# Kernel tuning notes

Hardware: AMD Instinct MI355X
Metric: run time of the kernel (lower is better)

## Reference

```python
import jax, jax.numpy as jnp
import numpy as np

VOCAB, D, S, T, B, E, C = 21128, 768, 50, 5, 512, 128, 10


def gcn(x, edges, W, b):
    # GCNConv with self-loops and symmetric normalization. x: [S, D]
    N = x.shape[0]
    loop = jnp.arange(N)
    src = jnp.concatenate([edges[0], loop])
    dst = jnp.concatenate([edges[1], loop])
    deg = jax.ops.segment_sum(jnp.ones_like(src, dtype=x.dtype), dst, num_segments=N)
    dinv = jax.lax.rsqrt(jnp.maximum(deg, 1e-12))
    norm = dinv[src] * dinv[dst]
    h = x @ W  # [S, 10]
    out = jax.ops.segment_sum(h[src] * norm[:, None], dst, num_segments=N)
    return out + b


def mpm(self_f, cross_f, assign, W1, b1, W2, b2):
    # multi-perspective matching, broadcast over leading dims; node dim = -2
    a = assign * self_f
    c = assign * cross_f
    num = jnp.sum(a * c, axis=-1)
    den = jnp.maximum(jnp.linalg.norm(a, axis=-1) * jnp.linalg.norm(c, axis=-1), 1e-8)
    cos = num / den
    bshape = jnp.broadcast_shapes(self_f.shape[:-2], cross_f.shape[:-2])
    sf = jnp.broadcast_to(self_f, bshape + self_f.shape[-2:])
    h = jnp.concatenate([cos[..., None], sf], axis=-1)  # [..., S, 11]
    h = jax.nn.relu(h @ W1 + b1) @ W2 + b2  # [..., S, 20]
    return jnp.max(h, axis=-2)  # [..., 20]


def setup_inputs() -> dict:
    key = jax.random.key(0)
    ks = jax.random.split(key, 20)
    inp = {
        "context_input": jax.random.randint(ks[0], (B, T, S), 0, VOCAB),
        "response_input": jax.random.randint(ks[1], (B, S), 0, VOCAB),
        "context_graph_adjs": jax.random.randint(ks[2], (B, T, 2, E), 0, S),
        "response_graph_adj": jax.random.randint(ks[3], (B, 2, E), 0, S),
        "word_emb": jax.random.normal(ks[4], (VOCAB, D), jnp.float32) * 0.02,
        "conv_W": jax.random.normal(ks[5], (D, C), jnp.float32) * 0.05,
        "conv_b": jnp.zeros((C,), jnp.float32),
        "cross_w": jax.random.uniform(ks[6], (D, C), jnp.float32),
        "attention_coef": jax.random.uniform(ks[7], (S, S), jnp.float32),
        "assign_weight": jax.random.uniform(ks[8], (S, C), jnp.float32),
        "mp_W1": jax.random.normal(ks[9], (C + 1, 20), jnp.float32) * 0.3,
        "mp_b1": jnp.zeros((20,), jnp.float32),
        "mp_W2": jax.random.normal(ks[10], (20, 20), jnp.float32) * 0.2,
        "mp_b2": jnp.zeros((20,), jnp.float32),
        "ffn_W1": jax.random.normal(ks[11], (80, 40), jnp.float32) * 0.1,
        "ffn_b1": jnp.zeros((40,), jnp.float32),
        "ffn_W2": jax.random.normal(ks[12], (40, 1), jnp.float32) * 0.2,
        "ffn_b2": jnp.zeros((1,), jnp.float32),
    }
    return inp


def reference(context_input, response_input, context_graph_adjs, response_graph_adj,
              word_emb, conv_W, conv_b, cross_w, attention_coef, assign_weight,
              mp_W1, mp_b1, mp_W2, mp_b2, ffn_W1, ffn_b1, ffn_W2, ffn_b2):
    ctx = word_emb[context_input]      # [B, T, S, D]
    resp = word_emb[response_input]    # [B, S, D]

    gcn_b = jax.vmap(gcn, in_axes=(0, 0, None, None))
    resp_gcn = gcn_b(resp, response_graph_adj, conv_W, conv_b)                      # [B, S, C]
    ctx_gcn = jax.vmap(gcn_b, in_axes=(0, 0, None, None))(ctx, context_graph_adjs, conv_W, conv_b)  # [B, T, S, C]

    # cross features: utterance cross comes from response, response cross from utterance
    u_cross = jnp.einsum('ps,bsk->bpk', attention_coef, resp @ cross_w)   # [B, S, C]
    r_cross = jnp.einsum('ps,btsk->btpk', attention_coef, ctx @ cross_w)  # [B, T, S, C]

    g_u = mpm(ctx_gcn, u_cross[:, None], assign_weight, mp_W1, mp_b1, mp_W2, mp_b2)       # [B, T, 20]
    g_r = mpm(resp_gcn[:, None], r_cross, assign_weight, mp_W1, mp_b1, mp_W2, mp_b2)      # [B, T, 20]

    feat = jnp.concatenate([g_u, g_r, g_u * g_r, jnp.abs(g_u - g_r)], axis=-1)  # [B, T, 80]
    logits = jax.nn.relu(feat @ ffn_W1 + ffn_b1) @ ffn_W2 + ffn_b2              # [B, T, 1]
    return jax.nn.sigmoid(jnp.sum(logits, axis=1))                              # [B, 1]
```

## Files before the change

### kernel.cpp

```cpp
#include <hip/hip_runtime.h>
#include <math.h>

#define VOCAB 21128
#define DD 768
#define SS 50
#define TT 5
#define BB 512
#define EE 128
#define CC 10
#define V20 (VOCAB * 20)
#define NG 2560
#define NALL 3072

__global__ void k_prep(const float* __restrict__ att, float* __restrict__ attG) {
    int i = blockIdx.x * 64 + threadIdx.x;
    if (i < SS * SS) {
        int p = i / SS, s = i - p * SS;
        attG[s * 52 + p] = att[i];
    }
}

__global__ __launch_bounds__(512) void k_vocab(const float* __restrict__ emb,
                                               const float* __restrict__ Wconv,
                                               const float* __restrict__ Wcross,
                                               float* __restrict__ hvp) {
    __shared__ float tile[8][64][21];
    const int wv = threadIdx.x >> 6, lane = threadIdx.x & 63;
    const int rowbase = blockIdx.x * 64;
    const int rsub = lane >> 2, m = lane & 3;

    const int d0w = blockIdx.y * 384 + __builtin_amdgcn_readfirstlane(wv * 48);

    float4 v[12];
#pragma unroll
    for (int ch = 0; ch < 3; ++ch) {
#pragma unroll
        for (int it = 0; it < 4; ++it) {
            int row = it * 16 + rsub;
            long r = rowbase + row;
            if (r >= VOCAB) r = VOCAB - 1;
            v[ch * 4 + it] = *(const float4*)(emb + r * DD + d0w + ch * 16 + m * 4);
        }
    }

    float acc[20];
#pragma unroll
    for (int c = 0; c < 20; c++) acc[c] = 0.f;

#pragma unroll
    for (int ch = 0; ch < 3; ++ch) {
        const int d0 = d0w + ch * 16;
#pragma unroll
        for (int it = 0; it < 4; ++it) {
            const int row = it * 16 + rsub;
            const float4 w = v[ch * 4 + it];
            tile[wv][row][m * 4 + 0] = w.x;
            tile[wv][row][m * 4 + 1] = w.y;
            tile[wv][row][m * 4 + 2] = w.z;
            tile[wv][row][m * 4 + 3] = w.w;
        }
#pragma unroll
        for (int d = 0; d < 16; ++d) {
            float e = tile[wv][lane][d];
            const float* wc = Wconv + (d0 + d) * 10;
            const float* wx = Wcross + (d0 + d) * 10;
#pragma unroll
            for (int c = 0; c < 10; c++) {
                acc[c] = fmaf(e, wc[c], acc[c]);
                acc[10 + c] = fmaf(e, wx[c], acc[10 + c]);
            }
        }
    }

    __syncthreads();
    float* pp = &tile[0][0][0];
#pragma unroll
    for (int c = 0; c < 20; c++) pp[wv * 1280 + lane * 20 + c] = acc[c];
    __syncthreads();
    float* outp = hvp + (long)blockIdx.y * V20;
    for (int i = threadIdx.x; i < 1280; i += 512) {
        int row = i / 20;
        long r = rowbase + row;
        if (r < VOCAB) {
            float s = 0.f;
#pragma unroll
            for (int w = 0; w < 8; ++w) s += pp[w * 1280 + i];
            outp[r * 20 + (i - row * 20)] = s;
        }
    }
}

__global__ __launch_bounds__(256) void k_gcn(const int* __restrict__ ctok,
                                             const int* __restrict__ cadj,
                                             const int* __restrict__ rtok,
                                             const int* __restrict__ radj,
                                             const float* __restrict__ hvp,
                                             const float* __restrict__ convb,
                                             const float* __restrict__ attG,
                                             float* __restrict__ P) {
    __shared__ float hcv[4][SS][12];
    __shared__ float hcx[4][SS][12];
    __shared__ float aggL[4][SS][11];
    __shared__ int dgS[4][64];
    const int tid = threadIdx.x, wv = tid >> 6, lane = tid & 63;
    const int G = blockIdx.x * 4 + wv;

    const int* tb;
    const int* ab;
    if (G < NG) { tb = ctok + (long)G * SS; ab = cadj + (long)G * 2 * EE; }
    else        { int b = G - NG; tb = rtok + (long)b * SS; ab = radj + (long)b * 2 * EE; }

    const int e1s = ab[lane], e2s = ab[lane + 64];
    const int e1d = ab[EE + lane], e2d = ab[EE + lane + 64];
    const int myTok = (lane < SS) ? tb[lane] : 0;

    dgS[wv][lane] = 0;
    atomicAdd(&dgS[wv][e1d], 1);
    atomicAdd(&dgS[wv][e2d], 1);

    const float4* hv4 = (const float4*)hvp;
#pragma unroll
    for (int it = 0; it < 4; ++it) {
        const int idx = it * 64 + lane;
        int row = idx / 5;
        const int q = idx - row * 5;
        const int rowc = (row < SS) ? row : (SS - 1);
        const int t = __shfl(myTok, rowc);
        if (idx < SS * 5) {
            const float4 a = hv4[(long)t * 5 + q];
            const float4 b = hv4[(long)(VOCAB * 5) + (long)t * 5 + q];
            const float4 w = make_float4(a.x + b.x, a.y + b.y, a.z + b.z, a.w + b.w);
            if (q == 0)      *(float4*)&hcv[wv][row][0] = w;
            else if (q == 1) *(float4*)&hcv[wv][row][4] = w;
            else if (q == 2) { hcv[wv][row][8] = w.x; hcv[wv][row][9] = w.y;
                               hcx[wv][row][0] = w.z; hcx[wv][row][1] = w.w; }
            else if (q == 3) { *(float2*)&hcx[wv][row][2] = make_float2(w.x, w.y);
                               *(float2*)&hcx[wv][row][4] = make_float2(w.z, w.w); }
            else             { *(float2*)&hcx[wv][row][6] = make_float2(w.x, w.y);
                               *(float2*)&hcx[wv][row][8] = make_float2(w.z, w.w); }
        }
    }

    float dv = 0.f;
    if (lane < SS) dv = rsqrtf((float)(dgS[wv][lane] + 1));

    float* aggW = &aggL[wv][0][0];
    for (int i = lane; i < SS * 11; i += 64) aggW[i] = 0.f;
    const float n1 = __shfl(dv, e1s) * __shfl(dv, e1d);
    const float n2 = __shfl(dv, e2s) * __shfl(dv, e2d);
#pragma unroll
    for (int c = 0; c < CC; c++) atomicAdd(&aggW[e1d * 11 + c], hcv[wv][e1s][c] * n1);
#pragma unroll
    for (int c = 0; c < CC; c++) atomicAdd(&aggW[e2d * 11 + c], hcv[wv][e2s][c] * n2);

    const int pc = (lane < SS) ? lane : (SS - 1);
    float xo[CC];
#pragma unroll
    for (int c = 0; c < CC; c++) xo[c] = hcx[wv][pc][c];

    const int p = lane;
    if (p < SS) {
        float gcn[CC];
        const float dp2 = dv * dv;
        const float4 s0 = *(const float4*)&hcv[wv][p][0];
        const float4 s1 = *(const float4*)&hcv[wv][p][4];
        const float s8 = hcv[wv][p][8], s9 = hcv[wv][p][9];
        gcn[0] = aggW[p * 11 + 0] + s0.x * dp2 + convb[0];
        gcn[1] = aggW[p * 11 + 1] + s0.y * dp2 + convb[1];
        gcn[2] = aggW[p * 11 + 2] + s0.z * dp2 + convb[2];
        gcn[3] = aggW[p * 11 + 3] + s0.w * dp2 + convb[3];
        gcn[4] = aggW[p * 11 + 4] + s1.x * dp2 + convb[4];
        gcn[5] = aggW[p * 11 + 5] + s1.y * dp2 + convb[5];
        gcn[6] = aggW[p * 11 + 6] + s1.z * dp2 + convb[6];
        gcn[7] = aggW[p * 11 + 7] + s1.w * dp2 + convb[7];
        gcn[8] = aggW[p * 11 + 8] + s8 * dp2 + convb[8];
        gcn[9] = aggW[p * 11 + 9] + s9 * dp2 + convb[9];

        float ax[CC];
#pragma unroll
        for (int c = 0; c < CC; c++) ax[c] = 0.f;
#pragma unroll 5
        for (int s = 0; s < SS; ++s) {
            const float a = attG[s * 52 + p];
#pragma unroll
            for (int c = 0; c < CC; c++) {
                const float xs = __uint_as_float(
                    __builtin_amdgcn_readlane(__float_as_uint(xo[c]), s));
                ax[c] = fmaf(a, xs, ax[c]);
            }
        }
        float4* o4 = (float4*)(P + (long)G * 1000 + p * 20);
        o4[0] = make_float4(gcn[0], gcn[1], gcn[2], gcn[3]);
        o4[1] = make_float4(gcn[4], gcn[5], gcn[6], gcn[7]);
        o4[2] = make_float4(gcn[8], gcn[9], ax[0], ax[1]);
        o4[3] = make_float4(ax[2], ax[3], ax[4], ax[5]);
        o4[4] = make_float4(ax[6], ax[7], ax[8], ax[9]);
    }
}

__global__ __launch_bounds__(640) void k_mpmf(const float* __restrict__ P,
                                              const float* __restrict__ assign,
                                              const float* __restrict__ W1, const float* __restrict__ b1,
                                              const float* __restrict__ W2, const float* __restrict__ b2,
                                              const float* __restrict__ fW1, const float* __restrict__ fb1,
                                              const float* __restrict__ fW2, const float* __restrict__ fb2,
                                              float* __restrict__ out) {
    __shared__ float W2T[20][21];
    __shared__ float asgL[SS][11];
    __shared__ float h1L[10][SS][20];
    __shared__ float guS[TT][20];
    __shared__ float grS[TT][20];
    __shared__ float fsum[256];
    const int tid = threadIdx.x, wv = tid >> 6, lane = tid & 63;
    const int b = blockIdx.x;
    const int t = wv >> 1, which = wv & 1;
    const int g = b * TT + t;

    for (int i = tid; i < 400; i += 640) W2T[i % 20][i / 20] = W2[i];
    for (int i = tid; i < SS * CC; i += 640) asgL[i / CC][i % CC] = assign[i];
    __syncthreads();

    const float* Pc = P + (long)g * 1000;
    const float* Pr = P + (long)(NG + b) * 1000;
    const float* selfP = which ? Pr : Pc;
    const float* croP  = which ? Pc : Pr;

    const int p = lane;
    float self[CC], cro[CC];
    if (p < SS) {
        const float4* s4 = (const float4*)(selfP + p * 20);
        const float4 a0 = s4[0], a1 = s4[1], a2 = s4[2];
        self[0] = a0.x; self[1] = a0.y; self[2] = a0.z; self[3] = a0.w;
        self[4] = a1.x; self[5] = a1.y; self[6] = a1.z; self[7] = a1.w;
        self[8] = a2.x; self[9] = a2.y;
        const float4* c4 = (const float4*)(croP + p * 20);
        const float4 b0 = c4[2], b1q = c4[3], b2q = c4[4];
        cro[0] = b0.z; cro[1] = b0.w;
        cro[2] = b1q.x; cro[3] = b1q.y; cro[4] = b1q.z; cro[5] = b1q.w;
        cro[6] = b2q.x; cro[7] = b2q.y; cro[8] = b2q.z; cro[9] = b2q.w;
    }

    const int j = lane % 20;
    const int grp = lane / 20;
    float w2r[20];
#pragma unroll
    for (int k = 0; k < 20; k++) w2r[k] = W2T[j][k];

    if (p < SS) {
        float num = 0.f, na = 0.f, nc2 = 0.f;
#pragma unroll
        for (int c = 0; c < CC; c++) {
            float av = asgL[p][c];
            float a = av * self[c];
            float cx = av * cro[c];
            num = fmaf(a, cx, num);
            na = fmaf(a, a, na);
            nc2 = fmaf(cx, cx, nc2);
        }
        float cosv = num / fmaxf(sqrtf(na) * sqrtf(nc2), 1e-8f);
        float h1[20];
#pragma unroll
        for (int q = 0; q < 20; q++) h1[q] = fmaf(cosv, W1[q], b1[q]);
#pragma unroll
        for (int k = 0; k < CC; k++) {
            float sv = self[k];
#pragma unroll
            for (int q = 0; q < 20; q++) h1[q] = fmaf(sv, W1[(k + 1) * 20 + q], h1[q]);
        }
        float4* hw = (float4*)&h1L[wv][p][0];
        hw[0] = make_float4(fmaxf(h1[0], 0.f), fmaxf(h1[1], 0.f), fmaxf(h1[2], 0.f), fmaxf(h1[3], 0.f));
        hw[1] = make_float4(fmaxf(h1[4], 0.f), fmaxf(h1[5], 0.f), fmaxf(h1[6], 0.f), fmaxf(h1[7], 0.f));
        hw[2] = make_float4(fmaxf(h1[8], 0.f), fmaxf(h1[9], 0.f), fmaxf(h1[10], 0.f), fmaxf(h1[11], 0.f));
        hw[3] = make_float4(fmaxf(h1[12], 0.f), fmaxf(h1[13], 0.f), fmaxf(h1[14], 0.f), fmaxf(h1[15], 0.f));
        hw[4] = make_float4(fmaxf(h1[16], 0.f), fmaxf(h1[17], 0.f), fmaxf(h1[18], 0.f), fmaxf(h1[19], 0.f));
    }

    float part = -1e30f;
    if (grp < 3) {
        const int s0 = grp * 17;
        const int s1 = (grp == 2) ? SS : (s0 + 17);
        for (int s = s0; s < s1; ++s) {
            const float* hr = &h1L[wv][s][0];
            float tt = 0.f;
#pragma unroll
            for (int k = 0; k < 20; k++) tt = fmaf(hr[k], w2r[k], tt);
            part = fmaxf(part, tt);
        }
    }
    const float a0 = __shfl(part, j);
    const float a1 = __shfl(part, j + 20);
    const float a2 = __shfl(part, j + 40);
    if (lane < 20) {
        float h2 = fmaxf(fmaxf(a0, a1), a2) + b2[lane];
        (which ? grS[t] : guS[t])[lane] = h2;
    }
    __syncthreads();

    float term = 0.f;
    if (tid < 200) {
        const int tt = tid / 40, jj = tid - tt * 40;
        float hvv = fb1[jj];
#pragma unroll
        for (int k = 0; k < 20; k++) {
            float u = guS[tt][k], r = grS[tt][k];
            hvv = fmaf(u, fW1[k * 40 + jj], hvv);
            hvv = fmaf(r, fW1[(20 + k) * 40 + jj], hvv);
            hvv = fmaf(u * r, fW1[(40 + k) * 40 + jj], hvv);
            hvv = fmaf(fabsf(u - r), fW1[(60 + k) * 40 + jj], hvv);
        }
        term = fmaxf(hvv, 0.f) * fW2[jj];
    }
    if (tid < 256) fsum[tid] = term;
    __syncthreads();
    if (wv == 0) {
        float s = fsum[lane] + fsum[lane + 64] + fsum[lane + 128] + fsum[lane + 192];
#pragma unroll
        for (int o = 32; o; o >>= 1) s += __shfl_xor(s, o);
        if (lane == 0) out[b] = 1.f / (1.f + expf(-(s + (float)TT * fb2[0])));
    }
}

extern "C" void kernel_launch(void* const* d_in, const int* in_sizes, int n_in,
                              void* d_out, int out_size, void* d_ws, size_t ws_size,
                              hipStream_t stream) {
    (void)in_sizes; (void)n_in; (void)out_size; (void)ws_size;
    const int* ctx_tok = (const int*)d_in[0];
    const int* resp_tok = (const int*)d_in[1];
    const int* ctx_adj = (const int*)d_in[2];
    const int* resp_adj = (const int*)d_in[3];
    const float* emb = (const float*)d_in[4];
    const float* convW = (const float*)d_in[5];
    const float* convb = (const float*)d_in[6];
    const float* crossW = (const float*)d_in[7];
    const float* att = (const float*)d_in[8];
    const float* assign = (const float*)d_in[9];
    const float* mpW1 = (const float*)d_in[10];
    const float* mpb1 = (const float*)d_in[11];
    const float* mpW2 = (const float*)d_in[12];
    const float* mpb2 = (const float*)d_in[13];
    const float* fW1 = (const float*)d_in[14];
    const float* fb1 = (const float*)d_in[15];
    const float* fW2 = (const float*)d_in[16];
    const float* fb2 = (const float*)d_in[17];

    float* ws = (float*)d_ws;
    float* hvp = ws;
    float* P = hvp + 2 * V20;
    float* attG = P + (long)NALL * 1000;
    float* outf = (float*)d_out;

    hipLaunchKernelGGL(k_prep, dim3(40), dim3(64), 0, stream, att, attG);
    hipLaunchKernelGGL(k_vocab, dim3((VOCAB + 63) / 64, 2), dim3(512), 0, stream,
                       emb, convW, crossW, hvp);
    hipLaunchKernelGGL(k_gcn, dim3(NALL / 4), dim3(256), 0, stream,
                       ctx_tok, ctx_adj, resp_tok, resp_adj, hvp, convb, attG, P);
    hipLaunchKernelGGL(k_mpmf, dim3(BB), dim3(640), 0, stream,
                       P, assign, mpW1, mpb1, mpW2, mpb2, fW1, fb1, fW2, fb2, outf);
}
```

Baseline: 76.38 us.

## Split GCN kernel into aggregation and cross-attention kernels with per-channel-pair waves

The fused GCN kernel is split in two. k_agg computes only the GCN aggregation, with each lane loading its own token row directly instead of using a cooperative shuffle-based gather. A new k_cross kernel computes the attention-weighted cross features with one wave per (graph, channel pair), giving five times more waves and a shorter serial readlane/FMA chain per wave. This adds a kernel launch and re-gathers the token rows in the second kernel.

```diff
diff --git a/kernel.cpp b/kernel.cpp
--- a/kernel.cpp
+++ b/kernel.cpp
@@ -90,16 +90,14 @@
     }
 }
 
-__global__ __launch_bounds__(256) void k_gcn(const int* __restrict__ ctok,
+__global__ __launch_bounds__(256) void k_agg(const int* __restrict__ ctok,
                                              const int* __restrict__ cadj,
                                              const int* __restrict__ rtok,
                                              const int* __restrict__ radj,
                                              const float* __restrict__ hvp,
                                              const float* __restrict__ convb,
-                                             const float* __restrict__ attG,
                                              float* __restrict__ P) {
     __shared__ float hcv[4][SS][12];
-    __shared__ float hcx[4][SS][12];
     __shared__ float aggL[4][SS][11];
     __shared__ int dgS[4][64];
     const int tid = threadIdx.x, wv = tid >> 6, lane = tid & 63;
@@ -112,33 +110,28 @@
 
     const int e1s = ab[lane], e2s = ab[lane + 64];
     const int e1d = ab[EE + lane], e2d = ab[EE + lane + 64];
-    const int myTok = (lane < SS) ? tb[lane] : 0;
+
+    const int p = lane;
+    const int pc = (p < SS) ? p : (SS - 1);
+    const long t = tb[pc];
+    const float4* hv4 = (const float4*)hvp;
+
+    const float4 a0 = hv4[t * 5 + 0], b0 = hv4[(long)(VOCAB * 5) + t * 5 + 0];
+    const float4 a1 = hv4[t * 5 + 1], b1 = hv4[(long)(VOCAB * 5) + t * 5 + 1];
+    const float4 a2 = hv4[t * 5 + 2], b2 = hv4[(long)(VOCAB * 5) + t * 5 + 2];
+    float rowv[CC];
+    rowv[0] = a0.x + b0.x; rowv[1] = a0.y + b0.y; rowv[2] = a0.z + b0.z; rowv[3] = a0.w + b0.w;
+    rowv[4] = a1.x + b1.x; rowv[5] = a1.y + b1.y; rowv[6] = a1.z + b1.z; rowv[7] = a1.w + b1.w;
+    rowv[8] = a2.x + b2.x; rowv[9] = a2.y + b2.y;
 
     dgS[wv][lane] = 0;
     atomicAdd(&dgS[wv][e1d], 1);
     atomicAdd(&dgS[wv][e2d], 1);
 
-    const float4* hv4 = (const float4*)hvp;
-#pragma unroll
-    for (int it = 0; it < 4; ++it) {
-        const int idx = it * 64 + lane;
-        int row = idx / 5;
-        const int q = idx - row * 5;
-        const int rowc = (row < SS) ? row : (SS - 1);
-        const int t = __shfl(myTok, rowc);
-        if (idx < SS * 5) {
-            const float4 a = hv4[(long)t * 5 + q];
-            const float4 b = hv4[(long)(VOCAB * 5) + (long)t * 5 + q];
-            const float4 w = make_float4(a.x + b.x, a.y + b.y, a.z + b.z, a.w + b.w);
-            if (q == 0)      *(float4*)&hcv[wv][row][0] = w;
-            else if (q == 1) *(float4*)&hcv[wv][row][4] = w;
-            else if (q == 2) { hcv[wv][row][8] = w.x; hcv[wv][row][9] = w.y;
-                               hcx[wv][row][0] = w.z; hcx[wv][row][1] = w.w; }
-            else if (q == 3) { *(float2*)&hcx[wv][row][2] = make_float2(w.x, w.y);
-                               *(float2*)&hcx[wv][row][4] = make_float2(w.z, w.w); }
-            else             { *(float2*)&hcx[wv][row][6] = make_float2(w.x, w.y);
-                               *(float2*)&hcx[wv][row][8] = make_float2(w.z, w.w); }
-        }
+    if (p < SS) {
+        *(float4*)&hcv[wv][p][0] = make_float4(rowv[0], rowv[1], rowv[2], rowv[3]);
+        *(float4*)&hcv[wv][p][4] = make_float4(rowv[4], rowv[5], rowv[6], rowv[7]);
+        *(float2*)&hcv[wv][p][8] = make_float2(rowv[8], rowv[9]);
     }
 
     float dv = 0.f;
@@ -153,49 +146,48 @@
 #pragma unroll
     for (int c = 0; c < CC; c++) atomicAdd(&aggW[e2d * 11 + c], hcv[wv][e2s][c] * n2);
 
+    if (p < SS) {
+        const float dp2 = dv * dv;
+        float g0[CC];
+#pragma unroll
+        for (int c = 0; c < CC; c++) g0[c] = aggW[p * 11 + c] + rowv[c] * dp2 + convb[c];
+        float* o = P + (long)G * 1000 + p * 20;
+        *(float4*)(o + 0) = make_float4(g0[0], g0[1], g0[2], g0[3]);
+        *(float4*)(o + 4) = make_float4(g0[4], g0[5], g0[6], g0[7]);
+        *(float2*)(o + 8) = make_float2(g0[8], g0[9]);
+    }
+}
+
+__global__ __launch_bounds__(256) void k_cross(const int* __restrict__ ctok,
+                                               const int* __restrict__ rtok,
+                                               const float* __restrict__ hvp,
+                                               const float* __restrict__ attG,
+                                               float* __restrict__ P) {
+    const int tid = threadIdx.x, wv = tid >> 6, lane = tid & 63;
+    const int wid = blockIdx.x * 4 + wv;
+    const int g = wid / 5, cpair = wid - g * 5;
+    const int c0 = 10 + 2 * cpair;
+
+    const int* tb = (g < NG) ? (ctok + (long)g * SS) : (rtok + (long)(g - NG) * SS);
     const int pc = (lane < SS) ? lane : (SS - 1);
-    float xo[CC];
-#pragma unroll
-    for (int c = 0; c < CC; c++) xo[c] = hcx[wv][pc][c];
-
-    const int p = lane;
-    if (p < SS) {
-        float gcn[CC];
-        const float dp2 = dv * dv;
-        const float4 s0 = *(const float4*)&hcv[wv][p][0];
-        const float4 s1 = *(const float4*)&hcv[wv][p][4];
-        const float s8 = hcv[wv][p][8], s9 = hcv[wv][p][9];
-        gcn[0] = aggW[p * 11 + 0] + s0.x * dp2 + convb[0];
-        gcn[1] = aggW[p * 11 + 1] + s0.y * dp2 + convb[1];
-        gcn[2] = aggW[p * 11 + 2] + s0.z * dp2 + convb[2];
-        gcn[3] = aggW[p * 11 + 3] + s0.w * dp2 + convb[3];
-        gcn[4] = aggW[p * 11 + 4] + s1.x * dp2 + convb[4];
-        gcn[5] = aggW[p * 11 + 5] + s1.y * dp2 + convb[5];
-        gcn[6] = aggW[p * 11 + 6] + s1.z * dp2 + convb[6];
-        gcn[7] = aggW[p * 11 + 7] + s1.w * dp2 + convb[7];
-        gcn[8] = aggW[p * 11 + 8] + s8 * dp2 + convb[8];
-        gcn[9] = aggW[p * 11 + 9] + s9 * dp2 + convb[9];
-
-        float ax[CC];
-#pragma unroll
-        for (int c = 0; c < CC; c++) ax[c] = 0.f;
-#pragma unroll 5
-        for (int s = 0; s < SS; ++s) {
-            const float a = attG[s * 52 + p];
-#pragma unroll
-            for (int c = 0; c < CC; c++) {
-                const float xs = __uint_as_float(
-                    __builtin_amdgcn_readlane(__float_as_uint(xo[c]), s));
-                ax[c] = fmaf(a, xs, ax[c]);
-            }
-        }
-        float4* o4 = (float4*)(P + (long)G * 1000 + p * 20);
-        o4[0] = make_float4(gcn[0], gcn[1], gcn[2], gcn[3]);
-        o4[1] = make_float4(gcn[4], gcn[5], gcn[6], gcn[7]);
-        o4[2] = make_float4(gcn[8], gcn[9], ax[0], ax[1]);
-        o4[3] = make_float4(ax[2], ax[3], ax[4], ax[5]);
-        o4[4] = make_float4(ax[6], ax[7], ax[8], ax[9]);
-    }
+    const long t = tb[pc];
+
+    const float2 xa = *(const float2*)(hvp + t * 20 + c0);
+    const float2 xb = *(const float2*)(hvp + (long)V20 + t * 20 + c0);
+    const float x0 = xa.x + xb.x;
+    const float x1 = xa.y + xb.y;
+
+    float ax0 = 0.f, ax1 = 0.f;
+#pragma unroll 10
+    for (int s = 0; s < SS; ++s) {
+        const float a = attG[s * 52 + pc];
+        const float v0 = __uint_as_float(__builtin_amdgcn_readlane(__float_as_uint(x0), s));
+        const float v1 = __uint_as_float(__builtin_amdgcn_readlane(__float_as_uint(x1), s));
+        ax0 = fmaf(a, v0, ax0);
+        ax1 = fmaf(a, v1, ax1);
+    }
+    if (lane < SS)
+        *(float2*)(P + (long)g * 1000 + lane * 20 + c0) = make_float2(ax0, ax1);
 }
 
 __global__ __launch_bounds__(640) void k_mpmf(const float* __restrict__ P,
@@ -352,8 +344,10 @@
     hipLaunchKernelGGL(k_prep, dim3(40), dim3(64), 0, stream, att, attG);
     hipLaunchKernelGGL(k_vocab, dim3((VOCAB + 63) / 64, 2), dim3(512), 0, stream,
                        emb, convW, crossW, hvp);
-    hipLaunchKernelGGL(k_gcn, dim3(NALL / 4), dim3(256), 0, stream,
-                       ctx_tok, ctx_adj, resp_tok, resp_adj, hvp, convb, attG, P);
+    hipLaunchKernelGGL(k_agg, dim3(NALL / 4), dim3(256), 0, stream,
+                       ctx_tok, ctx_adj, resp_tok, resp_adj, hvp, convb, P);
+    hipLaunchKernelGGL(k_cross, dim3(NALL * 5 / 4), dim3(256), 0, stream,
+                       ctx_tok, resp_tok, hvp, attG, P);
     hipLaunchKernelGGL(k_mpmf, dim3(BB), dim3(640), 0, stream,
                        P, assign, mpW1, mpb1, mpW2, mpb2, fW1, fb1, fW2, fb2, outf);
 }
```

After: 87.56 us. 14.6% more time.
